# Kernel optimization log

Hardware: AMD Instinct MI355X
Metric: run time of the kernel (lower is better)

## Reference

```python
import jax, jax.numpy as jnp
import numpy as np

B, T, N, M = 128, 256, 512, 512


def setup_inputs() -> dict:
    key = jax.random.key(0)
    ks = jax.random.split(key, 8)
    s = 0.05
    return {
        "inputs": jax.random.normal(ks[0], (B, T, N), dtype=jnp.float32),
        "W_e_w": jax.random.normal(ks[1], (T, 2 * M), dtype=jnp.float32) * s,
        "W_e_b": jax.random.normal(ks[2], (T,), dtype=jnp.float32) * s,
        "U_e_w": jax.random.normal(ks[3], (T, T), dtype=jnp.float32) * s,
        "w_ih": jax.random.normal(ks[4], (4 * M, N), dtype=jnp.float32) * s,
        "w_hh": jax.random.normal(ks[5], (4 * M, M), dtype=jnp.float32) * s,
        "b_ih": jax.random.normal(ks[6], (4 * M,), dtype=jnp.float32) * s,
        "b_hh": jax.random.normal(ks[7], (4 * M,), dtype=jnp.float32) * s,
    }


def reference(inputs, W_e_w, W_e_b, U_e_w, w_ih, w_hh, b_ih, b_hh):
    b, t_len, n = inputs.shape
    m = w_hh.shape[1]
    # y = U_e(inputs.permute(0,2,1)) : (B, N, T); loop-invariant, hoisted.
    y = jnp.einsum('btn,st->bns', inputs, U_e_w)
    # e_k_t[b,i] = sum_j sum_k x[b,k] * y[b,j,k]  (x row-repeated over N)
    ysum = y.sum(axis=1)  # (B, T)

    xs = jnp.swapaxes(inputs, 0, 1)  # (T, B, N)

    def step(carry, x_t):
        h, c = carry
        hc = jnp.concatenate([h, c], axis=1)          # (B, 2M)
        xw = hc @ W_e_w.T + W_e_b                      # (B, T)
        e = jnp.sum(xw * ysum, axis=-1)                # (B,) constant over N
        alpha = jax.nn.softmax(jnp.broadcast_to(e[:, None], (b, n)), axis=1)
        wx = alpha * x_t                               # (B, N)
        gates = wx @ w_ih.T + b_ih + h @ w_hh.T + b_hh  # (B, 4M)
        i_g, f_g, g_g, o_g = jnp.split(gates, 4, axis=1)
        i_g = jax.nn.sigmoid(i_g)
        f_g = jax.nn.sigmoid(f_g)
        g_g = jnp.tanh(g_g)
        o_g = jax.nn.sigmoid(o_g)
        c_new = f_g * c + i_g * g_g
        h_new = o_g * jnp.tanh(c_new)
        return (h_new, c_new), h_new

    h0 = jnp.zeros((b, m), dtype=inputs.dtype)
    c0 = jnp.zeros((b, m), dtype=inputs.dtype)
    _, hs = jax.lax.scan(step, (h0, c0), xs)
    return jnp.swapaxes(hs, 0, 1)  # (B, T, M)
```

## Files before the change

### kernel.cpp

```cpp
#include <hip/hip_runtime.h>


typedef __attribute__((ext_vector_type(8))) __bf16 bf16x8;
typedef __attribute__((ext_vector_type(8))) unsigned short u16x8;
typedef __attribute__((ext_vector_type(4))) float f32x4;
typedef unsigned short ushort_t;

__device__ __forceinline__ unsigned short f2b(float f) {
  unsigned u = __builtin_bit_cast(unsigned, f);
  unsigned r = (u + 0x7FFFu + ((u >> 16) & 1u)) >> 16;
  return (unsigned short)r;
}
__device__ __forceinline__ float b2f(unsigned short s) {
  unsigned u = ((unsigned)s) << 16;
  return __builtin_bit_cast(float, u);
}
__device__ __forceinline__ float sigm(float x) { return 1.0f / (1.0f + __expf(-x)); }
__device__ __forceinline__ float tanh_f(float x) { return 1.0f - 2.0f / (__expf(2.0f * x) + 1.0f); }

#define VMCNT(n) asm volatile("s_waitcnt vmcnt(" #n ")" ::: "memory")

__device__ __forceinline__ void hload16(f32x4* dst, const ushort_t* p) {
  asm volatile("global_load_dwordx4 %0, %1, off sc0 sc1"
               : "=v"(*dst) : "v"(p) : "memory");
}
__device__ __forceinline__ void hstore2(ushort_t* p, unsigned v) {
  asm volatile("global_store_short %0, %1, off sc0 sc1"
               :: "v"(p), "v"(v) : "memory");
}
__device__ __forceinline__ void xload_f32(float* dst, const float* p) {
  asm volatile("global_load_dword %0, %1, off" : "=v"(*dst) : "v"(p) : "memory");
}
__device__ __forceinline__ void xload_bf(unsigned* dst, const ushort_t* p) {
  asm volatile("global_load_ushort %0, %1, off" : "=v"(*dst) : "v"(p) : "memory");
}

__global__ __launch_bounds__(256) void convert_kernel(
    const float* __restrict__ inp, const float* __restrict__ wih,
    const float* __restrict__ bih, const float* __restrict__ bhh,
    ushort_t* __restrict__ X, ushort_t* __restrict__ W, float* __restrict__ bias)
{
  int tid = blockIdx.x * 256 + threadIdx.x;
  int stride = gridDim.x * 256;
  const float s = 1.0f / 512.0f;
  for (int i = tid; i < (16777216 / 4); i += stride) {
    float4 v = reinterpret_cast<const float4*>(inp)[i];
    ushort4 o; o.x = f2b(v.x * s); o.y = f2b(v.y * s); o.z = f2b(v.z * s); o.w = f2b(v.w * s);
    reinterpret_cast<ushort4*>(X)[i] = o;
  }
  for (int i = tid; i < (1048576 / 4); i += stride) {
    float4 v = reinterpret_cast<const float4*>(wih)[i];
    ushort4 o; o.x = f2b(v.x); o.y = f2b(v.y); o.z = f2b(v.z); o.w = f2b(v.w);
    reinterpret_cast<ushort4*>(W)[i] = o;
  }
  for (int i = tid; i < 2048; i += stride) bias[i] = bih[i] + bhh[i];
}

template<bool XGBF>
__global__ __launch_bounds__(256) void gemm_xg_kernel(
    const ushort_t* __restrict__ X, const ushort_t* __restrict__ W,
    const float* __restrict__ bias, void* __restrict__ xg)
{
  __shared__ bf16x8 AsV[1024];
  __shared__ bf16x8 BsV[1024];
  ushort_t* As = (ushort_t*)AsV;
  ushort_t* Bs = (ushort_t*)BsV;

  int tid = threadIdx.x;
  int lane = tid & 63;
  int wv = tid >> 6;
  int wr = wv >> 1, wc = wv & 1;
  int ll = lane & 15;
  int kg = lane >> 4;
  int bm = blockIdx.x & 255;
  int bn = blockIdx.x >> 8;

  f32x4 acc[4][4];
#pragma unroll
  for (int i = 0; i < 4; ++i)
#pragma unroll
    for (int j = 0; j < 4; ++j) acc[i][j] = (f32x4){0.f, 0.f, 0.f, 0.f};

  for (int kt = 0; kt < 8; ++kt) {
#pragma unroll
    for (int it = 0; it < 4; ++it) {
      int i = it * 256 + tid;
      int row = i >> 3, ch = i & 7;
      int de = row * 64 + ((ch ^ (row & 7)) << 3);
      *reinterpret_cast<bf16x8*>(As + de) =
          *reinterpret_cast<const bf16x8*>(X + (size_t)(bm * 128 + row) * 512 + kt * 64 + ch * 8);
      *reinterpret_cast<bf16x8*>(Bs + de) =
          *reinterpret_cast<const bf16x8*>(W + (size_t)(bn * 128 + row) * 512 + kt * 64 + ch * 8);
    }
    __syncthreads();
#pragma unroll
    for (int kc = 0; kc < 2; ++kc) {
      int kch = kc * 4 + kg;
      bf16x8 a[4], b[4];
#pragma unroll
      for (int fi = 0; fi < 4; ++fi) {
        int row = wr * 64 + fi * 16 + ll;
        a[fi] = *reinterpret_cast<const bf16x8*>(As + row * 64 + ((kch ^ (row & 7)) << 3));
      }
#pragma unroll
      for (int fj = 0; fj < 4; ++fj) {
        int row = wc * 64 + fj * 16 + ll;
        b[fj] = *reinterpret_cast<const bf16x8*>(Bs + row * 64 + ((kch ^ (row & 7)) << 3));
      }
#pragma unroll
      for (int fi = 0; fi < 4; ++fi)
#pragma unroll
        for (int fj = 0; fj < 4; ++fj)
          acc[fi][fj] = __builtin_amdgcn_mfma_f32_16x16x32_bf16(a[fi], b[fj], acc[fi][fj], 0, 0, 0);
    }
    __syncthreads();
  }
#pragma unroll
  for (int fj = 0; fj < 4; ++fj) {
    int colj = bn * 128 + wc * 64 + fj * 16 + ll;
    float bv = bias[colj];
#pragma unroll
    for (int fi = 0; fi < 4; ++fi)
#pragma unroll
      for (int r = 0; r < 4; ++r) {
        int rowi = bm * 128 + wr * 64 + fi * 16 + kg * 4 + r;
        float v = acc[fi][fj][r] + bv;
        if constexpr (XGBF) ((ushort_t*)xg)[(size_t)rowi * 2048 + colj] = f2b(v);
        else                ((float*)xg)[(size_t)rowi * 2048 + colj] = v;
      }
  }
}

template<bool XGBF>
__global__ __launch_bounds__(256, 1) void lstm_rec_kernel(
    const float* __restrict__ whh, const void* __restrict__ xg,
    ushort_t* __restrict__ hbuf , float* __restrict__ out,
    unsigned* __restrict__ bars)
{
  int tid = threadIdx.x;
  int lane = tid & 63;
  int wv = tid >> 6;
  int wvb = wv >> 1, wvm = wv & 1;
  int gb = blockIdx.x >> 4;
  int gm = blockIdx.x & 15;
  int ll = lane & 15, kg = lane >> 4;
  int b0 = gb * 32 + wvb * 16;
  int m0 = gm * 32 + wvm * 16;

  bf16x8 bfr[4][16];
#pragma unroll
  for (int g = 0; g < 4; ++g) {
    const float* wrow = whh + (size_t)(g * 512 + m0 + ll) * 512;
#pragma unroll
    for (int ks = 0; ks < 16; ++ks) {
      const float4* wp = reinterpret_cast<const float4*>(wrow + ks * 32 + kg * 8);
      float4 lo = wp[0], hi = wp[1];
      u16x8 tbits;
      tbits[0] = f2b(lo.x); tbits[1] = f2b(lo.y); tbits[2] = f2b(lo.z); tbits[3] = f2b(lo.w);
      tbits[4] = f2b(hi.x); tbits[5] = f2b(hi.y); tbits[6] = f2b(hi.z); tbits[7] = f2b(hi.w);
      bfr[g][ks] = __builtin_bit_cast(bf16x8, tbits);
    }
  }

  float c[4] = {0.f, 0.f, 0.f, 0.f};
  unsigned* bar = bars + gb * 32;

  for (int t = 0; t < 256; ++t) {
    const ushort_t* hread = hbuf + (size_t)(t & 1) * 65536;
    const ushort_t* hrow = hread + (size_t)(b0 + ll) * 512 + kg * 8;

    f32x4 hraw[16];
#pragma unroll
    for (int ks = 0; ks < 16; ++ks) hload16(&hraw[ks], hrow + ks * 32);

    float xv[4][4];
    unsigned xb[4][4];
#pragma unroll
    for (int g = 0; g < 4; ++g)
#pragma unroll
      for (int r = 0; r < 4; ++r) {
        size_t idx = ((size_t)(b0 + kg * 4 + r) * 256 + t) * 2048 + (size_t)g * 512 + m0 + ll;
        if constexpr (XGBF) xload_bf(&xb[g][r], (const ushort_t*)xg + idx);
        else                xload_f32(&xv[g][r], (const float*)xg + idx);
      }

    f32x4 acc[4];
#pragma unroll
    for (int g = 0; g < 4; ++g) acc[g] = (f32x4){0.f, 0.f, 0.f, 0.f};

    VMCNT(24);
    __builtin_amdgcn_sched_barrier(0);
#pragma unroll
    for (int ks = 0; ks < 8; ++ks) {
      bf16x8 a = __builtin_bit_cast(bf16x8, hraw[ks]);
#pragma unroll
      for (int g = 0; g < 4; ++g)
        acc[g] = __builtin_amdgcn_mfma_f32_16x16x32_bf16(a, bfr[g][ks], acc[g], 0, 0, 0);
    }
    VMCNT(16);
    __builtin_amdgcn_sched_barrier(0);
#pragma unroll
    for (int ks = 8; ks < 16; ++ks) {
      bf16x8 a = __builtin_bit_cast(bf16x8, hraw[ks]);
#pragma unroll
      for (int g = 0; g < 4; ++g)
        acc[g] = __builtin_amdgcn_mfma_f32_16x16x32_bf16(a, bfr[g][ks], acc[g], 0, 0, 0);
    }
    VMCNT(0);
    __builtin_amdgcn_sched_barrier(0);

    ushort_t* hwrite = hbuf + (size_t)((t + 1) & 1) * 65536;
    float hv[4];
#pragma unroll
    for (int r = 0; r < 4; ++r) {
      float x0, x1, x2, x3;
      if constexpr (XGBF) { x0 = b2f(xb[0][r]); x1 = b2f(xb[1][r]); x2 = b2f(xb[2][r]); x3 = b2f(xb[3][r]); }
      else                { x0 = xv[0][r]; x1 = xv[1][r]; x2 = xv[2][r]; x3 = xv[3][r]; }
      float ig = sigm(acc[0][r] + x0);
      float fg = sigm(acc[1][r] + x1);
      float gg = tanh_f(acc[2][r] + x2);
      float og = sigm(acc[3][r] + x3);
      c[r] = fg * c[r] + ig * gg;
      hv[r] = og * tanh_f(c[r]);
      hstore2(hwrite + (size_t)(b0 + kg * 4 + r) * 512 + m0 + ll, (unsigned)f2b(hv[r]));
    }

    VMCNT(0);
#pragma unroll
    for (int r = 0; r < 4; ++r)
      __builtin_nontemporal_store(hv[r], out + ((size_t)(b0 + kg * 4 + r) * 256 + t) * 512 + m0 + ll);

    if (t < 255) {
      __builtin_amdgcn_s_barrier();
      if (tid == 0) {
        __hip_atomic_fetch_add(bar, 1u, __ATOMIC_RELAXED, __HIP_MEMORY_SCOPE_AGENT);
        unsigned tgt = 16u * (unsigned)(t + 1);
        while (__hip_atomic_load(bar, __ATOMIC_RELAXED, __HIP_MEMORY_SCOPE_AGENT) < tgt)
          __builtin_amdgcn_s_sleep(1);
      }
      __builtin_amdgcn_s_barrier();
    }
  }
}

extern "C" void kernel_launch(void* const* d_in, const int* in_sizes, int n_in,
                              void* d_out, int out_size, void* d_ws, size_t ws_size,
                              hipStream_t stream)
{
  const float* inputs = (const float*)d_in[0];
  const float* w_ih = (const float*)d_in[4];
  const float* w_hh = (const float*)d_in[5];
  const float* b_ih = (const float*)d_in[6];
  const float* b_hh = (const float*)d_in[7];
  float* out = (float*)d_out;
  char* ws = (char*)d_ws;

  const size_t xg_f32_bytes = (size_t)32768 * 2048 * 4;
  const size_t xg_bf_bytes  = (size_t)32768 * 2048 * 2;
  const size_t xbytes = (size_t)16777216 * 2;
  const size_t wbytes = (size_t)1048576 * 2;
  const size_t biasb  = 2048 * 4;
  const size_t hbytes = (size_t)2 * 128 * 512 * 2;
  const size_t barb   = 512;
  const size_t tail = xbytes + wbytes + biasb + hbytes + barb + 1024;

  bool f32p = ws_size >= xg_f32_bytes + tail;
  size_t xgb  = f32p ? xg_f32_bytes : xg_bf_bytes;
  size_t oX   = xgb;
  size_t oW   = oX + xbytes;
  size_t oB   = oW + wbytes;
  size_t oH   = (oB + biasb + 255) & ~(size_t)255;
  size_t oBar = oH + hbytes;

  hipMemsetAsync(ws + oH, 0, hbytes + barb, stream);

  convert_kernel<<<2048, 256, 0, stream>>>(inputs, w_ih, b_ih, b_hh,
      (ushort_t*)(ws + oX), (ushort_t*)(ws + oW), (float*)(ws + oB));

  if (f32p) {
    gemm_xg_kernel<false><<<4096, 256, 0, stream>>>(
        (const ushort_t*)(ws + oX), (const ushort_t*)(ws + oW), (const float*)(ws + oB), ws);
    lstm_rec_kernel<false><<<64, 256, 0, stream>>>(
        w_hh, ws, (ushort_t*)(ws + oH), out, (unsigned*)(ws + oBar));
  } else {
    gemm_xg_kernel<true><<<4096, 256, 0, stream>>>(
        (const ushort_t*)(ws + oX), (const ushort_t*)(ws + oW), (const float*)(ws + oB), ws);
    lstm_rec_kernel<true><<<64, 256, 0, stream>>>(
        w_hh, ws, (ushort_t*)(ws + oH), out, (unsigned*)(ws + oBar));
  }
  (void)in_sizes; (void)n_in; (void)out_size;
}
```

Measured before the change: 1.364 ms.

## Interleave two independent batch chains per block to overlap grid-barrier latency

Splits each block's 32 batch rows into two independent 16-row chains with separate arrival counters and runs them alternately each timestep, using 128-thread blocks that reuse the same recurrent weight fragments. While one chain waits on its cross-block counter, the other chain's compute can proceed, which is meant to hide global synchronization latency. It halves the waves per block and serializes the two chains' MFMA work. It also adds a bounded spin guard that could break out before peers have arrived.

```diff
diff --git a/kernel.cpp b/kernel.cpp
--- a/kernel.cpp
+++ b/kernel.cpp
@@ -28,7 +28,7 @@
   asm volatile("global_store_short %0, %1, off sc0 sc1"
                :: "v"(p), "v"(v) : "memory");
 }
-__device__ __forceinline__ void xload_f32(float* dst, const float* p) {
+__device__ __forceinline__ void xload_f32(unsigned* dst, const float* p) {
   asm volatile("global_load_dword %0, %1, off" : "=v"(*dst) : "v"(p) : "memory");
 }
 __device__ __forceinline__ void xload_bf(unsigned* dst, const ushort_t* p) {
@@ -132,20 +132,109 @@
 }
 
 template<bool XGBF>
-__global__ __launch_bounds__(256, 1) void lstm_rec_kernel(
+__device__ __forceinline__ void chain_step(
+    int t, const bf16x8 (&bfr)[4][16], float (&c)[4],
+    ushort_t* hbuf, float* out, const void* xg, unsigned* ctr,
+    int b0, int m0, int ll, int kg, int tid)
+{
+  if (tid == 0) {
+    unsigned tgt = 16u * (unsigned)t;
+    unsigned guard = 0;
+    while (__hip_atomic_load(ctr, __ATOMIC_RELAXED, __HIP_MEMORY_SCOPE_AGENT) < tgt) {
+      if (++guard > (1u << 15)) break;
+      __builtin_amdgcn_s_sleep(1);
+    }
+  }
+  __builtin_amdgcn_s_barrier();
+
+  const ushort_t* hrow = hbuf + (size_t)(t & 1) * 65536 + (size_t)(b0 + ll) * 512 + kg * 8;
+  f32x4 hraw[16];
+#pragma unroll
+  for (int ks = 0; ks < 16; ++ks) hload16(&hraw[ks], hrow + ks * 32);
+
+  size_t lanebase = (size_t)(b0 + kg * 4) * 524288 + (size_t)t * 2048 + m0 + ll;
+  unsigned xv[16];
+#pragma unroll
+  for (int g = 0; g < 4; ++g)
+#pragma unroll
+    for (int r = 0; r < 4; ++r) {
+      size_t off = lanebase + (size_t)r * 524288 + g * 512;
+      if constexpr (XGBF) xload_bf(&xv[g * 4 + r], (const ushort_t*)xg + off);
+      else                xload_f32(&xv[g * 4 + r], (const float*)xg + off);
+    }
+
+  f32x4 acc[4];
+#pragma unroll
+  for (int g = 0; g < 4; ++g) acc[g] = (f32x4){0.f, 0.f, 0.f, 0.f};
+  VMCNT(24);
+  __builtin_amdgcn_sched_barrier(0);
+#pragma unroll
+  for (int ks = 0; ks < 8; ++ks) {
+    bf16x8 a = __builtin_bit_cast(bf16x8, hraw[ks]);
+#pragma unroll
+    for (int g = 0; g < 4; ++g)
+      acc[g] = __builtin_amdgcn_mfma_f32_16x16x32_bf16(a, bfr[g][ks], acc[g], 0, 0, 0);
+  }
+  VMCNT(16);
+  __builtin_amdgcn_sched_barrier(0);
+#pragma unroll
+  for (int ks = 8; ks < 16; ++ks) {
+    bf16x8 a = __builtin_bit_cast(bf16x8, hraw[ks]);
+#pragma unroll
+    for (int g = 0; g < 4; ++g)
+      acc[g] = __builtin_amdgcn_mfma_f32_16x16x32_bf16(a, bfr[g][ks], acc[g], 0, 0, 0);
+  }
+  VMCNT(0);
+  __builtin_amdgcn_sched_barrier(0);
+
+  ushort_t* hw = hbuf + (size_t)((t + 1) & 1) * 65536;
+  float hv[4];
+#pragma unroll
+  for (int r = 0; r < 4; ++r) {
+    float x0, x1, x2, x3;
+    if constexpr (XGBF) {
+      x0 = b2f((ushort_t)xv[0 * 4 + r]); x1 = b2f((ushort_t)xv[1 * 4 + r]);
+      x2 = b2f((ushort_t)xv[2 * 4 + r]); x3 = b2f((ushort_t)xv[3 * 4 + r]);
+    } else {
+      x0 = __builtin_bit_cast(float, xv[0 * 4 + r]); x1 = __builtin_bit_cast(float, xv[1 * 4 + r]);
+      x2 = __builtin_bit_cast(float, xv[2 * 4 + r]); x3 = __builtin_bit_cast(float, xv[3 * 4 + r]);
+    }
+    float ig = sigm(acc[0][r] + x0);
+    float fg = sigm(acc[1][r] + x1);
+    float gg = tanh_f(acc[2][r] + x2);
+    float og = sigm(acc[3][r] + x3);
+    c[r] = fg * c[r] + ig * gg;
+    hv[r] = og * tanh_f(c[r]);
+    hstore2(hw + (size_t)(b0 + kg * 4 + r) * 512 + m0 + ll, (unsigned)f2b(hv[r]));
+  }
+
+  VMCNT(0);
+  __builtin_amdgcn_sched_barrier(0);
+  __builtin_amdgcn_s_barrier();
+  if (tid == 0)
+    __hip_atomic_fetch_add(ctr, 1u, __ATOMIC_RELAXED, __HIP_MEMORY_SCOPE_AGENT);
+#pragma unroll
+  for (int r = 0; r < 4; ++r)
+    __builtin_nontemporal_store(hv[r], out + ((size_t)(b0 + kg * 4 + r) * 256 + t) * 512 + m0 + ll);
+}
+
+template<bool XGBF>
+__global__ __launch_bounds__(128, 1) void lstm_rec_kernel(
     const float* __restrict__ whh, const void* __restrict__ xg,
     ushort_t* __restrict__ hbuf , float* __restrict__ out,
-    unsigned* __restrict__ bars)
+    unsigned* __restrict__ ctrs )
 {
   int tid = threadIdx.x;
   int lane = tid & 63;
-  int wv = tid >> 6;
-  int wvb = wv >> 1, wvm = wv & 1;
-  int gb = blockIdx.x >> 4;
+  int wvm = tid >> 6;
   int gm = blockIdx.x & 15;
+  int pr = blockIdx.x >> 4;
   int ll = lane & 15, kg = lane >> 4;
-  int b0 = gb * 32 + wvb * 16;
   int m0 = gm * 32 + wvm * 16;
+  int b0A = pr * 32;
+  int b0B = pr * 32 + 16;
+  unsigned* ctrA = ctrs + (pr * 2) * 32;
+  unsigned* ctrB = ctrs + (pr * 2 + 1) * 32;
 
   bf16x8 bfr[4][16];
 #pragma unroll
@@ -162,84 +251,12 @@
     }
   }
 
-  float c[4] = {0.f, 0.f, 0.f, 0.f};
-  unsigned* bar = bars + gb * 32;
+  float cA[4] = {0.f, 0.f, 0.f, 0.f};
+  float cB[4] = {0.f, 0.f, 0.f, 0.f};
 
   for (int t = 0; t < 256; ++t) {
-    const ushort_t* hread = hbuf + (size_t)(t & 1) * 65536;
-    const ushort_t* hrow = hread + (size_t)(b0 + ll) * 512 + kg * 8;
-
-    f32x4 hraw[16];
-#pragma unroll
-    for (int ks = 0; ks < 16; ++ks) hload16(&hraw[ks], hrow + ks * 32);
-
-    float xv[4][4];
-    unsigned xb[4][4];
-#pragma unroll
-    for (int g = 0; g < 4; ++g)
-#pragma unroll
-      for (int r = 0; r < 4; ++r) {
-        size_t idx = ((size_t)(b0 + kg * 4 + r) * 256 + t) * 2048 + (size_t)g * 512 + m0 + ll;
-        if constexpr (XGBF) xload_bf(&xb[g][r], (const ushort_t*)xg + idx);
-        else                xload_f32(&xv[g][r], (const float*)xg + idx);
-      }
-
-    f32x4 acc[4];
-#pragma unroll
-    for (int g = 0; g < 4; ++g) acc[g] = (f32x4){0.f, 0.f, 0.f, 0.f};
-
-    VMCNT(24);
-    __builtin_amdgcn_sched_barrier(0);
-#pragma unroll
-    for (int ks = 0; ks < 8; ++ks) {
-      bf16x8 a = __builtin_bit_cast(bf16x8, hraw[ks]);
-#pragma unroll
-      for (int g = 0; g < 4; ++g)
-        acc[g] = __builtin_amdgcn_mfma_f32_16x16x32_bf16(a, bfr[g][ks], acc[g], 0, 0, 0);
-    }
-    VMCNT(16);
-    __builtin_amdgcn_sched_barrier(0);
-#pragma unroll
-    for (int ks = 8; ks < 16; ++ks) {
-      bf16x8 a = __builtin_bit_cast(bf16x8, hraw[ks]);
-#pragma unroll
-      for (int g = 0; g < 4; ++g)
-        acc[g] = __builtin_amdgcn_mfma_f32_16x16x32_bf16(a, bfr[g][ks], acc[g], 0, 0, 0);
-    }
-    VMCNT(0);
-    __builtin_amdgcn_sched_barrier(0);
-
-    ushort_t* hwrite = hbuf + (size_t)((t + 1) & 1) * 65536;
-    float hv[4];
-#pragma unroll
-    for (int r = 0; r < 4; ++r) {
-      float x0, x1, x2, x3;
-      if constexpr (XGBF) { x0 = b2f(xb[0][r]); x1 = b2f(xb[1][r]); x2 = b2f(xb[2][r]); x3 = b2f(xb[3][r]); }
-      else                { x0 = xv[0][r]; x1 = xv[1][r]; x2 = xv[2][r]; x3 = xv[3][r]; }
-      float ig = sigm(acc[0][r] + x0);
-      float fg = sigm(acc[1][r] + x1);
-      float gg = tanh_f(acc[2][r] + x2);
-      float og = sigm(acc[3][r] + x3);
-      c[r] = fg * c[r] + ig * gg;
-      hv[r] = og * tanh_f(c[r]);
-      hstore2(hwrite + (size_t)(b0 + kg * 4 + r) * 512 + m0 + ll, (unsigned)f2b(hv[r]));
-    }
-
-    VMCNT(0);
-#pragma unroll
-    for (int r = 0; r < 4; ++r)
-      __builtin_nontemporal_store(hv[r], out + ((size_t)(b0 + kg * 4 + r) * 256 + t) * 512 + m0 + ll);
-
-    if (t < 255) {
-      __builtin_amdgcn_s_barrier();
-      if (tid == 0) {
-        __hip_atomic_fetch_add(bar, 1u, __ATOMIC_RELAXED, __HIP_MEMORY_SCOPE_AGENT);
-        unsigned tgt = 16u * (unsigned)(t + 1);
-        while (__hip_atomic_load(bar, __ATOMIC_RELAXED, __HIP_MEMORY_SCOPE_AGENT) < tgt)
-          __builtin_amdgcn_s_sleep(1);
-      }
-      __builtin_amdgcn_s_barrier();
-    }
+    chain_step<XGBF>(t, bfr, cA, hbuf, out, xg, ctrA, b0A, m0, ll, kg, tid);
+    chain_step<XGBF>(t, bfr, cB, hbuf, out, xg, ctrB, b0B, m0, ll, kg, tid);
   }
 }
 
@@ -261,8 +278,8 @@
   const size_t wbytes = (size_t)1048576 * 2;
   const size_t biasb  = 2048 * 4;
   const size_t hbytes = (size_t)2 * 128 * 512 * 2;
-  const size_t barb   = 512;
-  const size_t tail = xbytes + wbytes + biasb + hbytes + barb + 1024;
+  const size_t ctrb   = 1024;
+  const size_t tail = xbytes + wbytes + biasb + hbytes + ctrb + 1024;
 
   bool f32p = ws_size >= xg_f32_bytes + tail;
   size_t xgb  = f32p ? xg_f32_bytes : xg_bf_bytes;
@@ -270,9 +287,9 @@
   size_t oW   = oX + xbytes;
   size_t oB   = oW + wbytes;
   size_t oH   = (oB + biasb + 255) & ~(size_t)255;
-  size_t oBar = oH + hbytes;
-
-  hipMemsetAsync(ws + oH, 0, hbytes + barb, stream);
+  size_t oC   = oH + hbytes;
+
+  hipMemsetAsync(ws + oH, 0, hbytes + ctrb, stream);
 
   convert_kernel<<<2048, 256, 0, stream>>>(inputs, w_ih, b_ih, b_hh,
       (ushort_t*)(ws + oX), (ushort_t*)(ws + oW), (float*)(ws + oB));
@@ -280,13 +297,13 @@
   if (f32p) {
     gemm_xg_kernel<false><<<4096, 256, 0, stream>>>(
         (const ushort_t*)(ws + oX), (const ushort_t*)(ws + oW), (const float*)(ws + oB), ws);
-    lstm_rec_kernel<false><<<64, 256, 0, stream>>>(
-        w_hh, ws, (ushort_t*)(ws + oH), out, (unsigned*)(ws + oBar));
+    lstm_rec_kernel<false><<<64, 128, 0, stream>>>(
+        w_hh, ws, (ushort_t*)(ws + oH), out, (unsigned*)(ws + oC));
   } else {
     gemm_xg_kernel<true><<<4096, 256, 0, stream>>>(
         (const ushort_t*)(ws + oX), (const ushort_t*)(ws + oW), (const float*)(ws + oB), ws);
-    lstm_rec_kernel<true><<<64, 256, 0, stream>>>(
-        w_hh, ws, (ushort_t*)(ws + oH), out, (unsigned*)(ws + oBar));
+    lstm_rec_kernel<true><<<64, 128, 0, stream>>>(
+        w_hh, ws, (ushort_t*)(ws + oH), out, (unsigned*)(ws + oC));
   }
   (void)in_sizes; (void)n_in; (void)out_size;
 }
```

New measurement: 1.880 ms. 37.8% more time.
